# Performance work log

Hardware: AMD Instinct MI355X
Metric: run time of the kernel (lower is better)

The kernel has to match this reference:

```python
import jax, jax.numpy as jnp
import numpy as np
import math

B, D_MODEL, SEQ_LEN, EMB_DIM, ORDER = 4, 1024, 4096, 5, 64


def setup_inputs() -> dict:
    key = jax.random.key(0)
    ks = jax.random.split(key, 12)
    L = SEQ_LEN
    # PositionalEmbedding: z = [t, Re(e^{-i f w}), Im(e^{-i f w})]
    t = jnp.linspace(0.0, 1.0, L)[None, :, None]                      # [1,L,1]
    bands = (EMB_DIM - 1) // 2
    t_rescaled = jnp.linspace(0.0, L - 1, L)[None, :, None]           # [1,L,1]
    w = 2 * math.pi * t_rescaled / L
    f = jnp.linspace(1e-4, bands - 1, bands)[None, None]              # [1,1,bands]
    zc = jnp.exp(-1j * f * w.astype(jnp.complex64))                   # [1,L,bands]
    z = jnp.concatenate([t, zc.real, zc.imag], axis=-1)               # [1,L,EMB_DIM]
    # ExponentialModulation deltas (fast_decay_pct=0.3, slow_decay_pct=1.5, target=0.01)
    max_decay = math.log(0.01) / 0.3
    min_decay = math.log(0.01) / 1.5
    deltas = jnp.linspace(min_decay, max_decay, D_MODEL)[None, None]  # [1,1,D]
    s = 0.1  # small init scale for MLP weights
    return {
        "x": jax.random.normal(ks[0], (B, D_MODEL, SEQ_LEN), jnp.float32),
        "L": SEQ_LEN,
        "z": z.astype(jnp.float32),
        "t": t.astype(jnp.float32),
        "deltas": deltas.astype(jnp.float32),
        "W1": jax.random.normal(ks[1], (ORDER, EMB_DIM), jnp.float32) * s,
        "b1": jax.random.normal(ks[2], (ORDER,), jnp.float32) * s,
        "freq": jnp.ones((1, ORDER), jnp.float32),  # Sin freq, w=1
        "W2": jax.random.normal(ks[3], (ORDER, ORDER), jnp.float32) * s,
        "b2": jax.random.normal(ks[4], (ORDER,), jnp.float32) * s,
        "W3": jax.random.normal(ks[5], (ORDER, ORDER), jnp.float32) * s,
        "b3": jax.random.normal(ks[6], (ORDER,), jnp.float32) * s,
        "W4": jax.random.normal(ks[7], (D_MODEL, ORDER), jnp.float32) * s,
        "bias": jax.random.normal(ks[8], (D_MODEL,), jnp.float32),
    }


def reference(x, L, z, t, deltas, W1, b1, freq, W2, b2, W3, b3, W4, bias):
    # --- implicit filter MLP: z [1,L,E] -> k [1,L,D] ---
    zL, tL = z[:, :L], t[:, :L]
    h = jnp.sin(freq * (jnp.einsum('ble,oe->blo', zL, W1) + b1))
    h = jnp.sin(freq * (jnp.einsum('blo,po->blp', h, W2) + b2))
    h = jnp.sin(freq * (jnp.einsum('blo,po->blp', h, W3) + b3))
    h = jnp.einsum('blo,do->bld', h, W4)                # [1,L,D], no bias
    # --- exponential modulation ---
    decay = jnp.exp(-tL * jnp.abs(deltas))              # [1,L,D]
    h = h * decay
    k = h[0].T                                          # [D, L] per-channel filters
    # --- FFT causal conv: irfft(rfft(u)*rfft(k)/n, norm='forward') == plain circular conv on 2L ---
    n = 2 * L
    u_f = jnp.fft.rfft(x, n=n)                          # [B,D,L+1] complex
    k_f = jnp.fft.rfft(k, n=n)                          # [D,L+1]
    y = jnp.fft.irfft(u_f * k_f, n=n)[..., :L]          # [B,D,L]
    out = y + x * bias[:, None]                         # D.unsqueeze(-1) bias term, gelu=False
    return out.astype(x.dtype)
```

## Files before the change

### kernel.cpp

```cpp
#include <hip/hip_runtime.h>
#include <math.h>


#define PAD(i) ((i) + ((i) >> 3))
#define TWO_PI 6.2831853071795864769f

typedef float2 cplx;

__device__ __forceinline__ cplx cmul(cplx a, cplx b) {
    return make_float2(a.x * b.x - a.y * b.y, a.x * b.y + a.y * b.x);
}

__device__ __forceinline__ void dft8(cplx v[8], float sgn) {
    cplx t;
    t = v[1]; v[1] = v[4]; v[4] = t;
    t = v[3]; v[3] = v[6]; v[6] = t;
#pragma unroll
    for (int i = 0; i < 8; i += 2) {
        cplx a = v[i], b = v[i + 1];
        v[i]     = make_float2(a.x + b.x, a.y + b.y);
        v[i + 1] = make_float2(a.x - b.x, a.y - b.y);
    }
#pragma unroll
    for (int i = 0; i < 8; i += 4) {
        cplx a = v[i], b = v[i + 2];
        v[i]     = make_float2(a.x + b.x, a.y + b.y);
        v[i + 2] = make_float2(a.x - b.x, a.y - b.y);
        cplx c1 = v[i + 1], d = v[i + 3];
        cplx dt = make_float2(-sgn * d.y, sgn * d.x);
        v[i + 1] = make_float2(c1.x + dt.x, c1.y + dt.y);
        v[i + 3] = make_float2(c1.x - dt.x, c1.y - dt.y);
    }
    const float C = 0.70710678118654752440f;
    cplx a, b, bt;
    a = v[0]; b = v[4];
    v[0] = make_float2(a.x + b.x, a.y + b.y);
    v[4] = make_float2(a.x - b.x, a.y - b.y);
    a = v[1]; b = v[5]; bt = cmul(b, make_float2(C, sgn * C));
    v[1] = make_float2(a.x + bt.x, a.y + bt.y);
    v[5] = make_float2(a.x - bt.x, a.y - bt.y);
    a = v[2]; b = v[6]; bt = make_float2(-sgn * b.y, sgn * b.x);
    v[2] = make_float2(a.x + bt.x, a.y + bt.y);
    v[6] = make_float2(a.x - bt.x, a.y - bt.y);
    a = v[3]; b = v[7]; bt = cmul(b, make_float2(-C, sgn * C));
    v[3] = make_float2(a.x + bt.x, a.y + bt.y);
    v[7] = make_float2(a.x - bt.x, a.y - bt.y);
}

template <int NS>
__device__ __forceinline__ void fft_pass_ip(cplx* buf, int j, float sgn) {
    cplx v[8];
#pragma unroll
    for (int r = 0; r < 8; r++) v[r] = buf[PAD(j + (r << 9))];
    if (NS > 1) {
        int jm = j & (NS - 1);
        float ang = sgn * (TWO_PI / (float)(NS * 8)) * (float)jm;
#pragma unroll
        for (int r = 1; r < 8; r++) {
            float s, c;
            __sincosf(ang * (float)r, &s, &c);
            v[r] = cmul(v[r], make_float2(c, s));
        }
    }
    dft8(v, sgn);
    __syncthreads();
    int jm2 = j & (NS - 1);
    int base = ((j & ~(NS - 1)) << 3) + jm2;
#pragma unroll
    for (int r = 0; r < 8; r++) buf[PAD(base + r * NS)] = v[r];
    __syncthreads();
}

__device__ __forceinline__ void fft_pass1_fwd_regs(cplx* buf, int j, const cplx xv[4]) {
    cplx v[8];
#pragma unroll
    for (int r = 0; r < 4; r++) v[r] = xv[r];
#pragma unroll
    for (int r = 4; r < 8; r++) v[r] = make_float2(0.f, 0.f);
    dft8(v, -1.0f);
#pragma unroll
    for (int r = 0; r < 8; r++) buf[PAD(8 * j + r)] = v[r];
    __syncthreads();
}

__global__ __launch_bounds__(256) void mlp_kernel(
    const float* __restrict__ zin, const float* __restrict__ W1,
    const float* __restrict__ b1, const float* __restrict__ freq,
    const float* __restrict__ W2, const float* __restrict__ b2,
    const float* __restrict__ W3, const float* __restrict__ b3,
    float* __restrict__ h3T) {
    __shared__ float hs1[64][64];
    __shared__ float hs2[64][64];
    int tid = threadIdx.x;
    int l = tid & 63, w = tid >> 6;
    int lg = blockIdx.x * 64 + l;

    float zf[5];
#pragma unroll
    for (int e = 0; e < 5; e++) zf[e] = zin[lg * 5 + e];

#pragma unroll
    for (int i = 0; i < 16; i++) {
        int o = w * 16 + i;
        float a = b1[o];
#pragma unroll
        for (int e = 0; e < 5; e++) a += W1[o * 5 + e] * zf[e];
        hs1[o][l] = __sinf(freq[o] * a);
    }
    __syncthreads();

    float acc[16];
#pragma unroll
    for (int i = 0; i < 16; i++) acc[i] = b2[w * 16 + i];
#pragma unroll 8
    for (int o = 0; o < 64; o++) {
        float hv = hs1[o][l];
#pragma unroll
        for (int i = 0; i < 16; i++) acc[i] += W2[(w * 16 + i) * 64 + o] * hv;
    }
#pragma unroll
    for (int i = 0; i < 16; i++)
        hs2[w * 16 + i][l] = __sinf(freq[w * 16 + i] * acc[i]);
    __syncthreads();

#pragma unroll
    for (int i = 0; i < 16; i++) acc[i] = b3[w * 16 + i];
#pragma unroll 8
    for (int o = 0; o < 64; o++) {
        float hv = hs2[o][l];
#pragma unroll
        for (int i = 0; i < 16; i++) acc[i] += W3[(w * 16 + i) * 64 + o] * hv;
    }
#pragma unroll
    for (int i = 0; i < 16; i++)
        h3T[(size_t)(w * 16 + i) * 4096 + lg] = __sinf(freq[w * 16 + i] * acc[i]);
}

__global__ __launch_bounds__(256) void kgemm_kernel(
    const float* __restrict__ h3T, const float* __restrict__ W4,
    const float* __restrict__ tvec, const float* __restrict__ deltas,
    float* __restrict__ kout) {
    int lt = blockIdx.x & 3;
    int dt = blockIdx.x >> 2;
    int l0 = lt * 1024 + threadIdx.x * 4;
    float4 acc[16];
#pragma unroll
    for (int i = 0; i < 16; i++) acc[i] = make_float4(0.f, 0.f, 0.f, 0.f);
#pragma unroll 8
    for (int o = 0; o < 64; o++) {
        float4 h = *(const float4*)(h3T + (size_t)o * 4096 + l0);
#pragma unroll
        for (int i = 0; i < 16; i++) {
            float wv = W4[(size_t)(dt * 16 + i) * 64 + o];
            acc[i].x += wv * h.x; acc[i].y += wv * h.y;
            acc[i].z += wv * h.z; acc[i].w += wv * h.w;
        }
    }
    float4 tl = *(const float4*)(tvec + l0);
#pragma unroll
    for (int i = 0; i < 16; i++) {
        int d = dt * 16 + i;
        float da = fabsf(deltas[d]);
        float4 o;
        o.x = acc[i].x * __expf(-tl.x * da);
        o.y = acc[i].y * __expf(-tl.y * da);
        o.z = acc[i].z * __expf(-tl.z * da);
        o.w = acc[i].w * __expf(-tl.w * da);
        *(float4*)(kout + (size_t)d * 4096 + l0) = o;
    }
}

__global__ __launch_bounds__(512) void filter_fft_kernel(
    const float* __restrict__ kin, float2* __restrict__ Kf) {
    __shared__ cplx buf[4608];
    int d = blockIdx.x, t = threadIdx.x;

    const cplx* k2 = (const cplx*)(kin + (size_t)d * 4096);
    cplx xv[4];
#pragma unroll
    for (int r = 0; r < 4; r++) xv[r] = k2[t + (r << 9)];
    fft_pass1_fwd_regs(buf, t, xv);
    fft_pass_ip<8>(buf, t, -1.0f);
    fft_pass_ip<64>(buf, t, -1.0f);
    fft_pass_ip<512>(buf, t, -1.0f);

    const float scale = 1.0f / 4096.0f;
    float2* KfRow = Kf + (size_t)d * 4104;
#pragma unroll
    for (int i = 0; i < 4; i++) {
        int k = t + (i << 9);
        if (k == 0) {
            cplx z0 = buf[PAD(0)];
            KfRow[0]    = make_float2((z0.x + z0.y) * scale, 0.f);
            KfRow[4096] = make_float2((z0.x - z0.y) * scale, 0.f);
            cplx zm = buf[PAD(2048)];
            KfRow[2048] = make_float2(zm.x * scale, -zm.y * scale);
        } else {
            int k2i = 4096 - k;
            cplx Zk = buf[PAD(k)], Zq = buf[PAD(k2i)];
            cplx Fe = make_float2(0.5f * (Zk.x + Zq.x), 0.5f * (Zk.y - Zq.y));
            cplx Fo = make_float2(0.5f * (Zk.y + Zq.y), -0.5f * (Zk.x - Zq.x));
            float s, c;
            __sincosf(-TWO_PI * (float)k * (1.0f / 8192.0f), &s, &c);
            cplx WFo = cmul(make_float2(c, s), Fo);
            KfRow[k]   = make_float2((Fe.x + WFo.x) * scale, (Fe.y + WFo.y) * scale);
            KfRow[k2i] = make_float2((Fe.x - WFo.x) * scale, -(Fe.y - WFo.y) * scale);
        }
    }
}

__global__ __launch_bounds__(512) void conv_kernel(
    const float* __restrict__ x, const float2* __restrict__ Kf,
    const float* __restrict__ bias, float* __restrict__ out) {
    __shared__ cplx buf[4608];
    int rid = blockIdx.x;
    int d = rid & 1023;
    int t = threadIdx.x;

    const cplx* x2 = (const cplx*)(x + (size_t)rid * 4096);
    cplx xv[4];
#pragma unroll
    for (int r = 0; r < 4; r++) xv[r] = x2[t + (r << 9)];
    fft_pass1_fwd_regs(buf, t, xv);
    fft_pass_ip<8>(buf, t, -1.0f);
    fft_pass_ip<64>(buf, t, -1.0f);
    fft_pass_ip<512>(buf, t, -1.0f);

    const float2* KfRow = Kf + (size_t)d * 4104;
#pragma unroll
    for (int i = 0; i < 4; i++) {
        int k = t + (i << 9);
        if (k == 0) {
            cplx z0 = buf[PAD(0)];
            float U0 = z0.x + z0.y;
            float UN = z0.x - z0.y;
            float Y0 = U0 * KfRow[0].x;
            float YN = UN * KfRow[4096].x;
            buf[PAD(0)] = make_float2(0.5f * (Y0 + YN), 0.5f * (Y0 - YN));
            cplx zm = buf[PAD(2048)];
            cplx Um = make_float2(zm.x, -zm.y);
            cplx Ym = cmul(Um, KfRow[2048]);
            buf[PAD(2048)] = make_float2(Ym.x, -Ym.y);
        } else {
            int k2i = 4096 - k;
            cplx Zk = buf[PAD(k)], Zq = buf[PAD(k2i)];
            cplx K1 = KfRow[k], K2 = KfRow[k2i];
            cplx Fe = make_float2(0.5f * (Zk.x + Zq.x), 0.5f * (Zk.y - Zq.y));
            cplx Fo = make_float2(0.5f * (Zk.y + Zq.y), -0.5f * (Zk.x - Zq.x));
            float s, c;
            __sincosf(-TWO_PI * (float)k * (1.0f / 8192.0f), &s, &c);
            cplx WFo = cmul(make_float2(c, s), Fo);
            cplx U1 = make_float2(Fe.x + WFo.x, Fe.y + WFo.y);
            cplx U2 = make_float2(Fe.x - WFo.x, -(Fe.y - WFo.y));
            cplx Y1 = cmul(U1, K1);
            cplx Y2 = cmul(U2, K2);
            cplx FeY = make_float2(0.5f * (Y1.x + Y2.x), 0.5f * (Y1.y - Y2.y));
            cplx T   = make_float2(0.5f * (Y1.x - Y2.x), 0.5f * (Y1.y + Y2.y));
            cplx FoY = cmul(make_float2(c, -s), T);
            buf[PAD(k)]   = make_float2(FeY.x - FoY.y, FeY.y + FoY.x);
            buf[PAD(k2i)] = make_float2(FeY.x + FoY.y, FoY.x - FeY.y);
        }
    }
    __syncthreads();

    fft_pass_ip<1>(buf, t, 1.0f);
    fft_pass_ip<8>(buf, t, 1.0f);
    fft_pass_ip<64>(buf, t, 1.0f);
    {
        cplx v[8];
#pragma unroll
        for (int r = 0; r < 8; r++) v[r] = buf[PAD(t + (r << 9))];
        float ang = (TWO_PI / 4096.0f) * (float)t;
#pragma unroll
        for (int r = 1; r < 8; r++) {
            float s, c;
            __sincosf(ang * (float)r, &s, &c);
            v[r] = cmul(v[r], make_float2(c, s));
        }
        dft8(v, 1.0f);
        float bd = bias[d];
        cplx* o2 = (cplx*)(out + (size_t)rid * 4096);
#pragma unroll
        for (int r = 0; r < 4; r++) {
            int m = t + (r << 9);
            cplx o;
            o.x = v[r].x + xv[r].x * bd;
            o.y = v[r].y + xv[r].y * bd;
            o2[m] = o;
        }
    }
}

extern "C" void kernel_launch(void* const* d_in, const int* in_sizes, int n_in,
                              void* d_out, int out_size, void* d_ws, size_t ws_size,
                              hipStream_t stream) {
    const float* x      = (const float*)d_in[0];
    const float* zin    = (const float*)d_in[2];
    const float* tvec   = (const float*)d_in[3];
    const float* deltas = (const float*)d_in[4];
    const float* W1     = (const float*)d_in[5];
    const float* b1     = (const float*)d_in[6];
    const float* freq   = (const float*)d_in[7];
    const float* W2     = (const float*)d_in[8];
    const float* b2     = (const float*)d_in[9];
    const float* W3     = (const float*)d_in[10];
    const float* b3     = (const float*)d_in[11];
    const float* W4     = (const float*)d_in[12];
    const float* bias   = (const float*)d_in[13];
    float* out = (float*)d_out;

    float*  h3T = (float*)d_ws;
    float2* Kf  = (float2*)((char*)d_ws + (size_t)64 * 4096 * sizeof(float));
    float* kbuf = out + (size_t)3072 * 4096;

    mlp_kernel<<<64, 256, 0, stream>>>(zin, W1, b1, freq, W2, b2, W3, b3, h3T);
    kgemm_kernel<<<256, 256, 0, stream>>>(h3T, W4, tvec, deltas, kbuf);
    filter_fft_kernel<<<1024, 512, 0, stream>>>(kbuf, Kf);
    conv_kernel<<<4096, 512, 0, stream>>>(x, Kf, bias, out);
}
```

Measured before the change: 244.7 us.

## Switch 4096-point FFTs from radix-8 to radix-16 with fewer shared-memory passes

Replaces the four radix-8 passes in the filter and convolution FFTs with three radix-16 passes, using 256 threads per block that each hold 16 values. The last forward pass and the first inverse pass are fused through the real-FFT post/pre-processing, with part of the data kept in registers. Twiddles now come from one sincos plus repeated multiplication, and a constant table replaces per-element sincos. This cuts the number of shared-memory round trips, barriers and transcendental calls. The cost is higher register pressure, which may lower occupancy, and a small loss of twiddle accuracy from chained products.

After: 237.5 us. -3.0%, faster.

```diff
diff --git a/kernel.cpp b/kernel.cpp
--- a/kernel.cpp
+++ b/kernel.cpp
@@ -2,84 +2,123 @@
 #include <math.h>
 
 
-#define PAD(i) ((i) + ((i) >> 3))
 #define TWO_PI 6.2831853071795864769f
-
-typedef float2 cplx;
-
-__device__ __forceinline__ cplx cmul(cplx a, cplx b) {
-    return make_float2(a.x * b.x - a.y * b.y, a.x * b.y + a.y * b.x);
-}
-
-__device__ __forceinline__ void dft8(cplx v[8], float sgn) {
-    cplx t;
-    t = v[1]; v[1] = v[4]; v[4] = t;
-    t = v[3]; v[3] = v[6]; v[6] = t;
-#pragma unroll
-    for (int i = 0; i < 8; i += 2) {
-        cplx a = v[i], b = v[i + 1];
-        v[i]     = make_float2(a.x + b.x, a.y + b.y);
-        v[i + 1] = make_float2(a.x - b.x, a.y - b.y);
-    }
-#pragma unroll
-    for (int i = 0; i < 8; i += 4) {
-        cplx a = v[i], b = v[i + 2];
-        v[i]     = make_float2(a.x + b.x, a.y + b.y);
-        v[i + 2] = make_float2(a.x - b.x, a.y - b.y);
-        cplx c1 = v[i + 1], d = v[i + 3];
-        cplx dt = make_float2(-sgn * d.y, sgn * d.x);
-        v[i + 1] = make_float2(c1.x + dt.x, c1.y + dt.y);
-        v[i + 3] = make_float2(c1.x - dt.x, c1.y - dt.y);
-    }
-    const float C = 0.70710678118654752440f;
-    cplx a, b, bt;
-    a = v[0]; b = v[4];
-    v[0] = make_float2(a.x + b.x, a.y + b.y);
-    v[4] = make_float2(a.x - b.x, a.y - b.y);
-    a = v[1]; b = v[5]; bt = cmul(b, make_float2(C, sgn * C));
-    v[1] = make_float2(a.x + bt.x, a.y + bt.y);
-    v[5] = make_float2(a.x - bt.x, a.y - bt.y);
-    a = v[2]; b = v[6]; bt = make_float2(-sgn * b.y, sgn * b.x);
-    v[2] = make_float2(a.x + bt.x, a.y + bt.y);
-    v[6] = make_float2(a.x - bt.x, a.y - bt.y);
-    a = v[3]; b = v[7]; bt = cmul(b, make_float2(-C, sgn * C));
-    v[3] = make_float2(a.x + bt.x, a.y + bt.y);
-    v[7] = make_float2(a.x - bt.x, a.y - bt.y);
-}
-
-template <int NS>
-__device__ __forceinline__ void fft_pass_ip(cplx* buf, int j, float sgn) {
-    cplx v[8];
-#pragma unroll
-    for (int r = 0; r < 8; r++) v[r] = buf[PAD(j + (r << 9))];
+#define C8 0.70710678118654752440f
+#define PM(r) ((((r) & 3) << 2) | ((r) >> 2))
+
+typedef __attribute__((ext_vector_type(2))) float cplx;
+
+static __device__ __forceinline__ cplx mkc(float x, float y) { cplx c; c.x = x; c.y = y; return c; }
+static __device__ __forceinline__ cplx caddi(cplx a, cplx b) { return mkc(a.x - b.y, a.y + b.x); }
+static __device__ __forceinline__ cplx csubi(cplx a, cplx b) { return mkc(a.x + b.y, a.y - b.x); }
+static __device__ __forceinline__ cplx cmulv(cplx a, cplx b) {
+    return mkc(a.x * b.x - a.y * b.y, a.x * b.y + a.y * b.x);
+}
+static __device__ __forceinline__ cplx cmuljv(cplx a, cplx b) {
+    return mkc(a.x * b.x + a.y * b.y, a.x * b.y - a.y * b.x);
+}
+
+template <bool FWD>
+__device__ __forceinline__ void dft4(cplx& a, cplx& b, cplx& c, cplx& d) {
+    cplx t0 = a + c, t1 = a - c, t2 = b + d, t3 = b - d;
+    a = t0 + t2; c = t0 - t2;
+    if (FWD) { b = csubi(t1, t3); d = caddi(t1, t3); }
+    else     { b = caddi(t1, t3); d = csubi(t1, t3); }
+}
+
+template <bool FWD>
+__device__ __forceinline__ void dft16_stageBC(cplx v[16]) {
+    const float c1 = 0.92387953251128675613f, s1 = 0.38268343236508977173f;
+    const cplx W1 = FWD ? mkc(c1, -s1) : mkc(c1, s1);
+    const cplx W2 = FWD ? mkc(C8, -C8) : mkc(C8, C8);
+    const cplx W3 = FWD ? mkc(s1, -c1) : mkc(s1, c1);
+    const cplx W6 = FWD ? mkc(-C8, -C8) : mkc(-C8, C8);
+    const cplx W9 = FWD ? mkc(-c1, s1) : mkc(-c1, -s1);
+    v[5]  = cmulv(v[5],  W1);
+    v[9]  = cmulv(v[9],  W2);
+    v[13] = cmulv(v[13], W3);
+    v[6]  = cmulv(v[6],  W2);
+    v[10] = FWD ? mkc(v[10].y, -v[10].x) : mkc(-v[10].y, v[10].x);
+    v[14] = cmulv(v[14], W6);
+    v[7]  = cmulv(v[7],  W3);
+    v[11] = cmulv(v[11], W6);
+    v[15] = cmulv(v[15], W9);
+    dft4<FWD>(v[0],  v[1],  v[2],  v[3]);
+    dft4<FWD>(v[4],  v[5],  v[6],  v[7]);
+    dft4<FWD>(v[8],  v[9],  v[10], v[11]);
+    dft4<FWD>(v[12], v[13], v[14], v[15]);
+}
+
+template <bool FWD>
+__device__ __forceinline__ void dft16(cplx v[16]) {
+    dft4<FWD>(v[0], v[4], v[8],  v[12]);
+    dft4<FWD>(v[1], v[5], v[9],  v[13]);
+    dft4<FWD>(v[2], v[6], v[10], v[14]);
+    dft4<FWD>(v[3], v[7], v[11], v[15]);
+    dft16_stageBC<FWD>(v);
+}
+
+__device__ __forceinline__ void twiddle_powers16(float ang, cplx w[16]) {
+    float s, c;
+    __sincosf(ang, &s, &c);
+    w[1]  = mkc(c, s);
+    w[2]  = cmulv(w[1], w[1]);
+    w[3]  = cmulv(w[2], w[1]);
+    w[4]  = cmulv(w[2], w[2]);
+    w[5]  = cmulv(w[4], w[1]);
+    w[6]  = cmulv(w[3], w[3]);
+    w[7]  = cmulv(w[4], w[3]);
+    w[8]  = cmulv(w[4], w[4]);
+    w[9]  = cmulv(w[8], w[1]);
+    w[10] = cmulv(w[5], w[5]);
+    w[11] = cmulv(w[8], w[3]);
+    w[12] = cmulv(w[6], w[6]);
+    w[13] = cmulv(w[8], w[5]);
+    w[14] = cmulv(w[7], w[7]);
+    w[15] = cmulv(w[8], w[7]);
+}
+
+template <int NS, bool FWD>
+__device__ __forceinline__ void fft16_pass_ip(cplx* __restrict__ buf, int j) {
+    cplx* rp = buf + (j + (j >> 4));
+    cplx v[16];
+#pragma unroll
+    for (int r = 0; r < 16; r++) v[r] = rp[272 * r];
     if (NS > 1) {
         int jm = j & (NS - 1);
-        float ang = sgn * (TWO_PI / (float)(NS * 8)) * (float)jm;
-#pragma unroll
-        for (int r = 1; r < 8; r++) {
-            float s, c;
-            __sincosf(ang * (float)r, &s, &c);
-            v[r] = cmul(v[r], make_float2(c, s));
-        }
-    }
-    dft8(v, sgn);
-    __syncthreads();
-    int jm2 = j & (NS - 1);
-    int base = ((j & ~(NS - 1)) << 3) + jm2;
-#pragma unroll
-    for (int r = 0; r < 8; r++) buf[PAD(base + r * NS)] = v[r];
-    __syncthreads();
-}
-
-__device__ __forceinline__ void fft_pass1_fwd_regs(cplx* buf, int j, const cplx xv[4]) {
-    cplx v[8];
-#pragma unroll
-    for (int r = 0; r < 4; r++) v[r] = xv[r];
-#pragma unroll
-    for (int r = 4; r < 8; r++) v[r] = make_float2(0.f, 0.f);
-    dft8(v, -1.0f);
-#pragma unroll
-    for (int r = 0; r < 8; r++) buf[PAD(8 * j + r)] = v[r];
+        float ang = (FWD ? -1.0f : 1.0f) * (TWO_PI / (float)(NS * 16)) * (float)jm;
+        cplx w[16];
+        twiddle_powers16(ang, w);
+#pragma unroll
+        for (int r = 1; r < 16; r++) v[r] = cmulv(v[r], w[r]);
+    }
+    dft16<FWD>(v);
+    __syncthreads();
+    int base = ((j & ~(NS - 1)) << 4) + (j & (NS - 1));
+    cplx* wp = buf + (base + (base >> 4));
+#pragma unroll
+    for (int r = 0; r < 16; r++) {
+        const int off = (NS == 1) ? r : (NS == 16) ? (17 * r) : (272 * r);
+        wp[off] = v[PM(r)];
+    }
+    __syncthreads();
+}
+
+__device__ __forceinline__ void fft16_pass1_fwd_regs(cplx* __restrict__ buf, int j,
+                                                     const cplx xv[8]) {
+    cplx v[16];
+#pragma unroll
+    for (int n0 = 0; n0 < 4; n0++) {
+        cplx a = xv[n0], b = xv[n0 + 4];
+        v[n0]      = a + b;
+        v[n0 + 4]  = csubi(a, b);
+        v[n0 + 8]  = a - b;
+        v[n0 + 12] = caddi(a, b);
+    }
+    dft16_stageBC<true>(v);
+    cplx* wp = buf + 17 * j;
+#pragma unroll
+    for (int r = 0; r < 16; r++) wp[r] = v[PM(r)];
     __syncthreads();
 }
 
@@ -170,123 +209,233 @@
     }
 }
 
-__global__ __launch_bounds__(512) void filter_fft_kernel(
-    const float* __restrict__ kin, float2* __restrict__ Kf) {
-    __shared__ cplx buf[4608];
-    int d = blockIdx.x, t = threadIdx.x;
+#define W32_TABLE                                                             \
+    const cplx W32C[8] = {                                                    \
+        mkc(1.0f, 0.0f),                                                      \
+        mkc(0.98078528040323044913f, -0.19509032201612826785f),               \
+        mkc(0.92387953251128675613f, -0.38268343236508977173f),               \
+        mkc(0.83146961230254523708f, -0.55557023301960222474f),               \
+        mkc(0.70710678118654752440f, -0.70710678118654752440f),               \
+        mkc(0.55557023301960222474f, -0.83146961230254523708f),               \
+        mkc(0.38268343236508977173f, -0.92387953251128675613f),               \
+        mkc(0.19509032201612826785f, -0.98078528040323044913f)};
+
+__global__ __launch_bounds__(256) void filter_fft_kernel(
+    const float* __restrict__ kin, cplx* __restrict__ Kf) {
+    __shared__ cplx buf[4352];
+    int d = blockIdx.x, j = threadIdx.x;
 
     const cplx* k2 = (const cplx*)(kin + (size_t)d * 4096);
-    cplx xv[4];
-#pragma unroll
-    for (int r = 0; r < 4; r++) xv[r] = k2[t + (r << 9)];
-    fft_pass1_fwd_regs(buf, t, xv);
-    fft_pass_ip<8>(buf, t, -1.0f);
-    fft_pass_ip<64>(buf, t, -1.0f);
-    fft_pass_ip<512>(buf, t, -1.0f);
+    cplx xv[8];
+#pragma unroll
+    for (int r = 0; r < 8; r++) xv[r] = k2[j + (r << 8)];
+    fft16_pass1_fwd_regs(buf, j, xv);
+    fft16_pass_ip<16, true>(buf, j);
+
+    cplx zv[16];
+    {
+        cplx* rp = buf + (j + (j >> 4));
+#pragma unroll
+        for (int r = 0; r < 16; r++) zv[r] = rp[272 * r];
+        cplx w[16];
+        twiddle_powers16(-TWO_PI * (float)j * (1.0f / 4096.0f), w);
+#pragma unroll
+        for (int r = 1; r < 16; r++) zv[r] = cmulv(zv[r], w[r]);
+        dft16<true>(zv);
+    }
+    __syncthreads();
+
+#pragma unroll
+    for (int s = 0; s < 8; s++) buf[9 * j + s] = zv[PM(8 + s)];
+    __syncthreads();
 
     const float scale = 1.0f / 4096.0f;
-    float2* KfRow = Kf + (size_t)d * 4104;
-#pragma unroll
-    for (int i = 0; i < 4; i++) {
-        int k = t + (i << 9);
-        if (k == 0) {
-            cplx z0 = buf[PAD(0)];
-            KfRow[0]    = make_float2((z0.x + z0.y) * scale, 0.f);
-            KfRow[4096] = make_float2((z0.x - z0.y) * scale, 0.f);
-            cplx zm = buf[PAD(2048)];
-            KfRow[2048] = make_float2(zm.x * scale, -zm.y * scale);
-        } else {
-            int k2i = 4096 - k;
-            cplx Zk = buf[PAD(k)], Zq = buf[PAD(k2i)];
-            cplx Fe = make_float2(0.5f * (Zk.x + Zq.x), 0.5f * (Zk.y - Zq.y));
-            cplx Fo = make_float2(0.5f * (Zk.y + Zq.y), -0.5f * (Zk.x - Zq.x));
-            float s, c;
-            __sincosf(-TWO_PI * (float)k * (1.0f / 8192.0f), &s, &c);
-            cplx WFo = cmul(make_float2(c, s), Fo);
-            KfRow[k]   = make_float2((Fe.x + WFo.x) * scale, (Fe.y + WFo.y) * scale);
-            KfRow[k2i] = make_float2((Fe.x - WFo.x) * scale, -(Fe.y - WFo.y) * scale);
+    float sb, cb;
+    __sincosf(-TWO_PI * (float)j * (1.0f / 8192.0f), &sb, &cb);
+    cplx w0 = mkc(cb, sb);
+    W32_TABLE
+    cplx* KfRow = Kf + (size_t)d * 4104;
+    if (j == 0) {
+        cplx z0 = zv[PM(0)];
+        KfRow[0]    = mkc((z0.x + z0.y) * scale, 0.f);
+        KfRow[4096] = mkc((z0.x - z0.y) * scale, 0.f);
+        cplx zm = buf[0];
+        KfRow[2048] = mkc(zm.x * scale, -zm.y * scale);
+#pragma unroll
+        for (int i = 1; i < 8; i++) {
+            cplx Zk = zv[PM(i)];
+            cplx Zq = buf[8 - i];
+            cplx wk = cmulv(w0, W32C[i]);
+            cplx Fe = mkc(0.5f * (Zk.x + Zq.x), 0.5f * (Zk.y - Zq.y));
+            cplx Fo = mkc(0.5f * (Zk.y + Zq.y), 0.5f * (Zq.x - Zk.x));
+            cplx WFo = cmulv(wk, Fo);
+            KfRow[256 * i]        = scale * (Fe + WFo);
+            cplx t = Fe - WFo;
+            KfRow[4096 - 256 * i] = mkc(scale * t.x, -scale * t.y);
         }
-    }
-}
-
-__global__ __launch_bounds__(512) void conv_kernel(
-    const float* __restrict__ x, const float2* __restrict__ Kf,
+    } else {
+        int p = 256 - j;
+        cplx* kfp = KfRow + j;
+        cplx* kfq = KfRow + (4096 - j);
+#pragma unroll
+        for (int i = 0; i < 8; i++) {
+            cplx Zk = zv[PM(i)];
+            cplx Zq = buf[9 * p + 7 - i];
+            cplx wk = (i == 0) ? w0 : cmulv(w0, W32C[i]);
+            cplx Fe = mkc(0.5f * (Zk.x + Zq.x), 0.5f * (Zk.y - Zq.y));
+            cplx Fo = mkc(0.5f * (Zk.y + Zq.y), 0.5f * (Zq.x - Zk.x));
+            cplx WFo = cmulv(wk, Fo);
+            kfp[256 * i]  = scale * (Fe + WFo);
+            cplx t = Fe - WFo;
+            kfq[-256 * i] = mkc(scale * t.x, -scale * t.y);
+        }
+    }
+}
+
+__global__ __launch_bounds__(256) void conv_kernel(
+    const float* __restrict__ x, const cplx* __restrict__ Kf,
     const float* __restrict__ bias, float* __restrict__ out) {
-    __shared__ cplx buf[4608];
+    __shared__ cplx buf[4352];
     int rid = blockIdx.x;
     int d = rid & 1023;
-    int t = threadIdx.x;
+    int j = threadIdx.x;
 
     const cplx* x2 = (const cplx*)(x + (size_t)rid * 4096);
-    cplx xv[4];
-#pragma unroll
-    for (int r = 0; r < 4; r++) xv[r] = x2[t + (r << 9)];
-    fft_pass1_fwd_regs(buf, t, xv);
-    fft_pass_ip<8>(buf, t, -1.0f);
-    fft_pass_ip<64>(buf, t, -1.0f);
-    fft_pass_ip<512>(buf, t, -1.0f);
-
-    const float2* KfRow = Kf + (size_t)d * 4104;
-#pragma unroll
-    for (int i = 0; i < 4; i++) {
-        int k = t + (i << 9);
-        if (k == 0) {
-            cplx z0 = buf[PAD(0)];
-            float U0 = z0.x + z0.y;
-            float UN = z0.x - z0.y;
-            float Y0 = U0 * KfRow[0].x;
-            float YN = UN * KfRow[4096].x;
-            buf[PAD(0)] = make_float2(0.5f * (Y0 + YN), 0.5f * (Y0 - YN));
-            cplx zm = buf[PAD(2048)];
-            cplx Um = make_float2(zm.x, -zm.y);
-            cplx Ym = cmul(Um, KfRow[2048]);
-            buf[PAD(2048)] = make_float2(Ym.x, -Ym.y);
+    cplx xv[8];
+#pragma unroll
+    for (int r = 0; r < 8; r++) xv[r] = x2[j + (r << 8)];
+    fft16_pass1_fwd_regs(buf, j, xv);
+    fft16_pass_ip<16, true>(buf, j);
+
+    cplx zv[16];
+    {
+        cplx* rp = buf + (j + (j >> 4));
+#pragma unroll
+        for (int r = 0; r < 16; r++) zv[r] = rp[272 * r];
+        cplx w[16];
+        twiddle_powers16(-TWO_PI * (float)j * (1.0f / 4096.0f), w);
+#pragma unroll
+        for (int r = 1; r < 16; r++) zv[r] = cmulv(zv[r], w[r]);
+        dft16<true>(zv);
+    }
+    __syncthreads();
+
+#pragma unroll
+    for (int s = 0; s < 8; s++) buf[9 * j + s] = zv[PM(8 + s)];
+    __syncthreads();
+
+    cplx yl[8];
+    {
+        float sb, cb;
+        __sincosf(-TWO_PI * (float)j * (1.0f / 8192.0f), &sb, &cb);
+        cplx w0 = mkc(cb, sb);
+        W32_TABLE
+        const cplx* KfRow = Kf + (size_t)d * 4104;
+        if (j == 0) {
+            cplx z0 = zv[PM(0)];
+            float U0 = z0.x + z0.y, UN = z0.x - z0.y;
+            float Y0 = U0 * KfRow[0].x, YN = UN * KfRow[4096].x;
+            yl[0] = mkc(0.5f * (Y0 + YN), 0.5f * (Y0 - YN));
+            cplx zm = buf[0];
+            cplx Km = KfRow[2048];
+            cplx Ym = cmuljv(zm, Km);
+            buf[0] = mkc(Ym.x, -Ym.y);
+#pragma unroll
+            for (int i = 1; i < 8; i++) {
+                cplx Zk = zv[PM(i)];
+                cplx Zq = buf[8 - i];
+                cplx K1 = KfRow[256 * i], K2 = KfRow[4096 - 256 * i];
+                cplx wk = cmulv(w0, W32C[i]);
+                cplx Fe = mkc(0.5f * (Zk.x + Zq.x), 0.5f * (Zk.y - Zq.y));
+                cplx Fo = mkc(0.5f * (Zk.y + Zq.y), 0.5f * (Zq.x - Zk.x));
+                cplx WFo = cmulv(wk, Fo);
+                cplx U1 = Fe + WFo;
+                cplx U2 = mkc(Fe.x - WFo.x, WFo.y - Fe.y);
+                cplx Y1 = cmulv(U1, K1);
+                cplx Y2 = cmulv(U2, K2);
+                cplx FeY = mkc(0.5f * (Y1.x + Y2.x), 0.5f * (Y1.y - Y2.y));
+                cplx T   = mkc(0.5f * (Y1.x - Y2.x), 0.5f * (Y1.y + Y2.y));
+                cplx FoY = cmuljv(wk, T);
+                yl[i] = caddi(FeY, FoY);
+                buf[8 - i] = mkc(FeY.x + FoY.y, FoY.x - FeY.y);
+            }
         } else {
-            int k2i = 4096 - k;
-            cplx Zk = buf[PAD(k)], Zq = buf[PAD(k2i)];
-            cplx K1 = KfRow[k], K2 = KfRow[k2i];
-            cplx Fe = make_float2(0.5f * (Zk.x + Zq.x), 0.5f * (Zk.y - Zq.y));
-            cplx Fo = make_float2(0.5f * (Zk.y + Zq.y), -0.5f * (Zk.x - Zq.x));
-            float s, c;
-            __sincosf(-TWO_PI * (float)k * (1.0f / 8192.0f), &s, &c);
-            cplx WFo = cmul(make_float2(c, s), Fo);
-            cplx U1 = make_float2(Fe.x + WFo.x, Fe.y + WFo.y);
-            cplx U2 = make_float2(Fe.x - WFo.x, -(Fe.y - WFo.y));
-            cplx Y1 = cmul(U1, K1);
-            cplx Y2 = cmul(U2, K2);
-            cplx FeY = make_float2(0.5f * (Y1.x + Y2.x), 0.5f * (Y1.y - Y2.y));
-            cplx T   = make_float2(0.5f * (Y1.x - Y2.x), 0.5f * (Y1.y + Y2.y));
-            cplx FoY = cmul(make_float2(c, -s), T);
-            buf[PAD(k)]   = make_float2(FeY.x - FoY.y, FeY.y + FoY.x);
-            buf[PAD(k2i)] = make_float2(FeY.x + FoY.y, FoY.x - FeY.y);
+            int p = 256 - j;
+            const cplx* kfp = KfRow + j;
+            const cplx* kfq = KfRow + (4096 - j);
+#pragma unroll
+            for (int i = 0; i < 8; i++) {
+                cplx Zk = zv[PM(i)];
+                cplx Zq = buf[9 * p + 7 - i];
+                cplx K1 = kfp[256 * i], K2 = kfq[-256 * i];
+                cplx wk = (i == 0) ? w0 : cmulv(w0, W32C[i]);
+                cplx Fe = mkc(0.5f * (Zk.x + Zq.x), 0.5f * (Zk.y - Zq.y));
+                cplx Fo = mkc(0.5f * (Zk.y + Zq.y), 0.5f * (Zq.x - Zk.x));
+                cplx WFo = cmulv(wk, Fo);
+                cplx U1 = Fe + WFo;
+                cplx U2 = mkc(Fe.x - WFo.x, WFo.y - Fe.y);
+                cplx Y1 = cmulv(U1, K1);
+                cplx Y2 = cmulv(U2, K2);
+                cplx FeY = mkc(0.5f * (Y1.x + Y2.x), 0.5f * (Y1.y - Y2.y));
+                cplx T   = mkc(0.5f * (Y1.x - Y2.x), 0.5f * (Y1.y + Y2.y));
+                cplx FoY = cmuljv(wk, T);
+                yl[i] = caddi(FeY, FoY);
+                buf[9 * p + 7 - i] = mkc(FeY.x + FoY.y, FoY.x - FeY.y);
+            }
         }
     }
     __syncthreads();
 
-    fft_pass_ip<1>(buf, t, 1.0f);
-    fft_pass_ip<8>(buf, t, 1.0f);
-    fft_pass_ip<64>(buf, t, 1.0f);
+    cplx uv[16];
+#pragma unroll
+    for (int i = 0; i < 8; i++) uv[i] = yl[i];
+#pragma unroll
+    for (int s = 0; s < 8; s++) uv[8 + s] = buf[9 * j + s];
+    __syncthreads();
+    dft16<false>(uv);
     {
-        cplx v[8];
-#pragma unroll
-        for (int r = 0; r < 8; r++) v[r] = buf[PAD(t + (r << 9))];
-        float ang = (TWO_PI / 4096.0f) * (float)t;
-#pragma unroll
-        for (int r = 1; r < 8; r++) {
-            float s, c;
-            __sincosf(ang * (float)r, &s, &c);
-            v[r] = cmul(v[r], make_float2(c, s));
-        }
-        dft8(v, 1.0f);
+        cplx* wp = buf + 17 * j;
+#pragma unroll
+        for (int r = 0; r < 16; r++) wp[r] = uv[PM(r)];
+    }
+    __syncthreads();
+    fft16_pass_ip<16, false>(buf, j);
+
+    {
+        cplx* rp = buf + (j + (j >> 4));
+        cplx v[16];
+#pragma unroll
+        for (int r = 0; r < 16; r++) v[r] = rp[272 * r];
+        cplx w[16];
+        twiddle_powers16(TWO_PI * (float)j * (1.0f / 4096.0f), w);
+#pragma unroll
+        for (int r = 1; r < 16; r++) v[r] = cmulv(v[r], w[r]);
+        dft4<false>(v[0], v[4], v[8],  v[12]);
+        dft4<false>(v[1], v[5], v[9],  v[13]);
+        dft4<false>(v[2], v[6], v[10], v[14]);
+        dft4<false>(v[3], v[7], v[11], v[15]);
+        const float c1 = 0.92387953251128675613f, s1 = 0.38268343236508977173f;
+        v[5]  = cmulv(v[5],  mkc(c1, s1));
+        v[9]  = cmulv(v[9],  mkc(C8, C8));
+        v[13] = cmulv(v[13], mkc(s1, c1));
+        v[6]  = cmulv(v[6],  mkc(C8, C8));
+        v[10] = mkc(-v[10].y, v[10].x);
+        v[14] = cmulv(v[14], mkc(-C8, C8));
+        v[7]  = cmulv(v[7],  mkc(s1, c1));
+        v[11] = cmulv(v[11], mkc(-C8, C8));
+        v[15] = cmulv(v[15], mkc(-c1, -s1));
         float bd = bias[d];
         cplx* o2 = (cplx*)(out + (size_t)rid * 4096);
 #pragma unroll
-        for (int r = 0; r < 4; r++) {
-            int m = t + (r << 9);
-            cplx o;
-            o.x = v[r].x + xv[r].x * bd;
-            o.y = v[r].y + xv[r].y * bd;
-            o2[m] = o;
+        for (int m = 0; m < 4; m++) {
+            cplx t0 = v[4 * m] + v[4 * m + 2];
+            cplx t1 = v[4 * m] - v[4 * m + 2];
+            cplx t2 = v[4 * m + 1] + v[4 * m + 3];
+            cplx t3 = v[4 * m + 1] - v[4 * m + 3];
+            cplx Xa = t0 + t2;
+            cplx Xb = caddi(t1, t3);
+            o2[j + 256 * m]       = Xa + bd * xv[m];
+            o2[j + 256 * (m + 4)] = Xb + bd * xv[m + 4];
         }
     }
 }
@@ -309,12 +458,12 @@
     const float* bias   = (const float*)d_in[13];
     float* out = (float*)d_out;
 
-    float*  h3T = (float*)d_ws;
-    float2* Kf  = (float2*)((char*)d_ws + (size_t)64 * 4096 * sizeof(float));
+    float* h3T = (float*)d_ws;
+    cplx*  Kf  = (cplx*)((char*)d_ws + (size_t)64 * 4096 * sizeof(float));
     float* kbuf = out + (size_t)3072 * 4096;
 
     mlp_kernel<<<64, 256, 0, stream>>>(zin, W1, b1, freq, W2, b2, W3, b3, h3T);
     kgemm_kernel<<<256, 256, 0, stream>>>(h3T, W4, tvec, deltas, kbuf);
-    filter_fft_kernel<<<1024, 512, 0, stream>>>(kbuf, Kf);
-    conv_kernel<<<4096, 512, 0, stream>>>(x, Kf, bias, out);
-}
+    filter_fft_kernel<<<1024, 256, 0, stream>>>(kbuf, Kf);
+    conv_kernel<<<4096, 256, 0, stream>>>(x, Kf, bias, out);
+}
```
